# Kernel optimization log

Hardware: AMD Instinct MI355X
Metric: run time of the kernel (lower is better)

## Reference

```python
import jax, jax.numpy as jnp
import numpy as np
import math

D, NH, DFF = 1024, 16, 4096
B, S = 2, 2048
EPS = 1e-5


def _mha(q_in, k_in, v_in, wq, bq, wk, bk, wv, bv, wo, bo, mask):
    Bq, Sq, Dm = q_in.shape
    Sk = k_in.shape[1]
    dh = Dm // NH
    q = (q_in @ wq + bq).reshape(Bq, Sq, NH, dh).transpose(0, 2, 1, 3)
    k = (k_in @ wk + bk).reshape(Bq, Sk, NH, dh).transpose(0, 2, 1, 3)
    v = (v_in @ wv + bv).reshape(Bq, Sk, NH, dh).transpose(0, 2, 1, 3)
    scores = jnp.einsum('bhqd,bhkd->bhqk', q, k) / math.sqrt(dh)
    scores = jnp.where(mask == 0, jnp.float32(-1e9), scores)
    w = jax.nn.softmax(scores, axis=-1)
    out = jnp.einsum('bhqk,bhkd->bhqd', w, v)
    out = out.transpose(0, 2, 1, 3).reshape(Bq, Sq, Dm)
    return out @ wo + bo


def _ln(x, g, b):
    mu = jnp.mean(x, axis=-1, keepdims=True)
    var = jnp.var(x, axis=-1, keepdims=True)
    return (x - mu) * jax.lax.rsqrt(var + EPS) * g + b


def setup_inputs() -> dict:
    key = jax.random.key(0)
    ks = jax.random.split(key, 20)
    sc = 1.0 / math.sqrt(D)
    inp = {
        'x': jax.random.normal(ks[0], (B, S, D), jnp.float32),
        'encoder_output': jax.random.normal(ks[1], (B, S, D), jnp.float32),
        'src_mask': jnp.ones((B, 1, 1, S), jnp.int32),
        'tgt_mask': jnp.tril(jnp.ones((S, S), jnp.int32))[None, None],
    }
    names = ['s_wq', 's_wk', 's_wv', 's_wo', 'c_wq', 'c_wk', 'c_wv', 'c_wo']
    for i, n in enumerate(names):
        inp[n] = jax.random.normal(ks[2 + i], (D, D), jnp.float32) * sc
        inp[n.replace('w', 'b')] = jnp.zeros((D,), jnp.float32)
    inp['ff_w1'] = jax.random.normal(ks[10], (D, DFF), jnp.float32) * sc
    inp['ff_b1'] = jnp.zeros((DFF,), jnp.float32)
    inp['ff_w2'] = jax.random.normal(ks[11], (DFF, D), jnp.float32) / math.sqrt(DFF)
    inp['ff_b2'] = jnp.zeros((D,), jnp.float32)
    for i in (1, 2, 3):
        inp[f'ln{i}_g'] = jnp.ones((D,), jnp.float32)
        inp[f'ln{i}_b'] = jnp.zeros((D,), jnp.float32)
    return inp


def reference(x, encoder_output, src_mask, tgt_mask,
              s_wq, s_bq, s_wk, s_bk, s_wv, s_bv, s_wo, s_bo,
              c_wq, c_bq, c_wk, c_bk, c_wv, c_bv, c_wo, c_bo,
              ff_w1, ff_b1, ff_w2, ff_b2,
              ln1_g, ln1_b, ln2_g, ln2_b, ln3_g, ln3_b):
    # self-attention + residual + LN (dropout is identity in eval)
    a = _mha(x, x, x, s_wq, s_bq, s_wk, s_bk, s_wv, s_bv, s_wo, s_bo, tgt_mask)
    x = _ln(x + a, ln1_g, ln1_b)
    # cross-attention
    a = _mha(x, encoder_output, encoder_output,
             c_wq, c_bq, c_wk, c_bk, c_wv, c_bv, c_wo, c_bo, src_mask)
    x = _ln(x + a, ln2_g, ln2_b)
    # FFN
    f = jax.nn.relu(x @ ff_w1 + ff_b1) @ ff_w2 + ff_b2
    return _ln(x + f, ln3_g, ln3_b)
```

## Files before the change

kernel.cpp:

```cpp
#include <hip/hip_runtime.h>
#include <hip/hip_bf16.h>
#include <stdint.h>


#define DEV static __device__ __forceinline__

typedef short bf16s;
typedef __attribute__((ext_vector_type(8))) short bf16x8;
typedef __attribute__((ext_vector_type(4))) float f32x4;

DEV short f2b(float f) {
    union { __hip_bfloat16 h; short s; } u;
    u.h = __float2bfloat16(f);
    return u.s;
}

DEV unsigned pk2(float lo, float hi) {
    union { __hip_bfloat162 h; unsigned u; } u;
    u.h = __float22bfloat162_rn(float2{lo, hi});
    return u.u;
}

DEV f32x4 mfma16(bf16x8 a, bf16x8 b, f32x4 c) {
    return __builtin_amdgcn_mfma_f32_16x16x32_bf16(a, b, c, 0, 0, 0);
}

DEV void gload_lds16(const bf16s* g, short* l) {
    __builtin_amdgcn_global_load_lds(
        (const __attribute__((address_space(1))) void*)g,
        (__attribute__((address_space(3))) void*)l,
        16, 0, 0);
}

__global__ __launch_bounds__(256) void cast2_f32_bf16_kernel(
    const float* __restrict__ a, const float* __restrict__ b,
    bf16s* __restrict__ out, int n)
{
    int i = (blockIdx.x * 256 + threadIdx.x) * 8;
    const float* src = (i < n) ? a : b;
    int j = (i < n) ? i : i - n;
    const float4 u = *(const float4*)(src + j);
    const float4 v = *(const float4*)(src + j + 4);
    bf16x8 r;
    r[0] = f2b(u.x); r[1] = f2b(u.y); r[2] = f2b(u.z); r[3] = f2b(u.w);
    r[4] = f2b(v.x); r[5] = f2b(v.y); r[6] = f2b(v.z); r[7] = f2b(v.w);
    *(bf16x8*)(out + i) = r;
}

struct P8 { const float* p[8]; };

__global__ __launch_bounds__(256) void transpose_cast8_kernel(
    P8 srcs, bf16s* __restrict__ dst)
{
    __shared__ short tile[64][65];
    const float* W = srcs.p[blockIdx.z];
    bf16s* Wt = dst + (size_t)blockIdx.z * 1024 * 1024;
    const int n0 = blockIdx.x * 64, k0 = blockIdx.y * 64;
    const int t = threadIdx.x;
#pragma unroll
    for (int it = 0; it < 16; ++it) {
        int idx = it * 256 + t;
        int r = idx >> 6, c = idx & 63;
        tile[r][c] = f2b(W[(size_t)(k0 + r) * 1024 + n0 + c]);
    }
    __syncthreads();
#pragma unroll
    for (int it = 0; it < 16; ++it) {
        int idx = it * 256 + t;
        int r = idx >> 6, c = idx & 63;
        Wt[(size_t)(n0 + r) * 1024 + k0 + c] = tile[c][r];
    }
}

__global__ __launch_bounds__(256) void transpose_cast_kernel(
    const float* __restrict__ W, bf16s* __restrict__ Wt, int Krows, int Ncols)
{
    __shared__ short tile[64][65];
    const int n0 = blockIdx.x * 64, k0 = blockIdx.y * 64;
    const int t = threadIdx.x;
#pragma unroll
    for (int it = 0; it < 16; ++it) {
        int idx = it * 256 + t;
        int r = idx >> 6, c = idx & 63;
        tile[r][c] = f2b(W[(size_t)(k0 + r) * Ncols + n0 + c]);
    }
    __syncthreads();
#pragma unroll
    for (int it = 0; it < 16; ++it) {
        int idx = it * 256 + t;
        int r = idx >> 6, c = idx & 63;
        Wt[(size_t)(n0 + r) * Krows + k0 + c] = tile[c][r];
    }
}

__global__ __launch_bounds__(256) void transpose_v_kernel(
    const bf16s* __restrict__ V, int ldv, bf16s* __restrict__ Vt, int Sk)
{
    __shared__ short tile[64][65];
    const int s0 = blockIdx.x * 64;
    const int bh = blockIdx.y, b = bh >> 4, h = bh & 15;
    const int t = threadIdx.x;
#pragma unroll
    for (int it = 0; it < 16; ++it) {
        int idx = it * 256 + t;
        int r = idx >> 6, c = idx & 63;
        tile[r][c] = V[(size_t)(b * Sk + s0 + r) * ldv + h * 64 + c];
    }
    __syncthreads();
#pragma unroll
    for (int it = 0; it < 16; ++it) {
        int idx = it * 256 + t;
        int r = idx >> 6, c = idx & 63;
        Vt[((size_t)bh * 64 + r) * Sk + s0 + c] = tile[c][r];
    }
}

__global__ void concat3_kernel(const float* a, const float* b, const float* c,
                               float* o, int n)
{
    int i = blockIdx.x * 256 + threadIdx.x;
    if (i < n) { o[i] = a[i]; o[n + i] = b[i]; o[2 * n + i] = c[i]; }
}
__global__ void concat2_kernel(const float* a, const float* b, float* o, int n)
{
    int i = blockIdx.x * 256 + threadIdx.x;
    if (i < n) { o[i] = a[i]; o[n + i] = b[i]; }
}

template<int BM, int OUT_BF16, int RELU>
__global__ __launch_bounds__(256, (BM == 64 ? 4 : 2))
void gemm_bt_kernel(const bf16s* __restrict__ A, const bf16s* __restrict__ Bt,
                    const float* __restrict__ bias, void* __restrict__ Cp,
                    int M, int N, int K)
{
    constexpr int BN = 128;
    constexpr int WR = BM / 64;
    constexpr int WC = 4 / WR;
    constexpr int TN = BN / WC;
    constexpr int NF = TN / 16;
    constexpr int RA = BM / 64;
    constexpr int ASZ = BM * 32;

    __shared__ short As[2 * ASZ];
    __shared__ short Bs[2 * BN * 32];

    const int t = threadIdx.x, lane = t & 63, wave = t >> 6;
    const int g = lane >> 4, ln16 = lane & 15;
    const int wr = wave / WC, wc = wave % WC;
    const int rowA0 = blockIdx.y * BM, rowB0 = blockIdx.x * BN;

    const bf16s* Ab = A + (size_t)rowA0 * K;
    const bf16s* Bb = Bt + (size_t)rowB0 * K;

    f32x4 acc[4][NF] = {};

    auto stage = [&](int buf, int k0) {
        short* Ad = As + buf * ASZ;
        short* Bd = Bs + buf * BN * 32;
#pragma unroll
        for (int rnd = 0; rnd < RA; ++rnd) {
            int p = rnd * 256 + t;
            int sr = p >> 3, c3 = (p & 7) ^ (sr & 7);
            int r = sr * 2 + (c3 >> 2), c = c3 & 3;
            gload_lds16(Ab + (size_t)r * K + k0 + c * 8,
                        Ad + (rnd * 256 + wave * 64) * 8);
        }
#pragma unroll
        for (int rnd = 0; rnd < 2; ++rnd) {
            int p = rnd * 256 + t;
            int sr = p >> 3, c3 = (p & 7) ^ (sr & 7);
            int r = sr * 2 + (c3 >> 2), c = c3 & 3;
            gload_lds16(Bb + (size_t)r * K + k0 + c * 8,
                        Bd + (rnd * 256 + wave * 64) * 8);
        }
    };

    stage(0, 0);
    __syncthreads();
    int cur = 0;
    for (int k0 = 0; k0 < K; k0 += 32) {
        if (k0 + 32 < K) stage(cur ^ 1, k0 + 32);
        const short* Ar = As + cur * ASZ;
        const short* Br = Bs + cur * BN * 32;
        bf16x8 af[4], bfr[NF];
#pragma unroll
        for (int m = 0; m < 4; ++m) {
            int r = wr * 64 + m * 16 + ln16;
            int sr = r >> 1, c3 = (r & 1) * 4 + g;
            af[m] = *(const bf16x8*)(Ar + sr * 64 + ((c3 ^ (sr & 7)) * 8));
        }
#pragma unroll
        for (int n = 0; n < NF; ++n) {
            int r = wc * TN + n * 16 + ln16;
            int sr = r >> 1, c3 = (r & 1) * 4 + g;
            bfr[n] = *(const bf16x8*)(Br + sr * 64 + ((c3 ^ (sr & 7)) * 8));
        }
#pragma unroll
        for (int m = 0; m < 4; ++m)
#pragma unroll
            for (int n = 0; n < NF; ++n)
                acc[m][n] = mfma16(af[m], bfr[n], acc[m][n]);
        __syncthreads();
        cur ^= 1;
    }

    const int row0 = rowA0 + wr * 64, col0 = rowB0 + wc * TN;
#pragma unroll
    for (int n = 0; n < NF; ++n) {
        const int col = col0 + n * 16 + ln16;
        const float bv = bias[col];
#pragma unroll
        for (int m = 0; m < 4; ++m) {
#pragma unroll
            for (int r = 0; r < 4; ++r) {
                int row = row0 + m * 16 + g * 4 + r;
                float v = acc[m][n][r] + bv;
                if (RELU) v = fmaxf(v, 0.f);
                if (OUT_BF16) ((bf16s*)Cp)[(size_t)row * N + col] = f2b(v);
                else          ((float*)Cp)[(size_t)row * N + col] = v;
            }
        }
    }
}

template<int CAUSAL>
__global__ __launch_bounds__(256, 4)
void flash_kernel(const bf16s* __restrict__ Q, int ldq,
                  const bf16s* __restrict__ K, int ldk,
                  const bf16s* __restrict__ Vt,
                  bf16s* __restrict__ O, int ldo,
                  int Sq, int Sk, float scale)
{
    __shared__ short Ks[2 * 64 * 64];
    __shared__ short Vs[2 * 64 * 64];
    __shared__ short Ps[4 * 16 * 64];
    const int t = threadIdx.x, lane = t & 63, wave = t >> 6;
    const int g = lane >> 4, ln16 = lane & 15;
    const int qt = CAUSAL ? (int)(gridDim.x - 1 - blockIdx.x) : (int)blockIdx.x;
    const int bh = blockIdx.y, b = bh >> 4, h = bh & 15;
    const int q0 = qt * 64;
    const float sc2 = scale * 1.44269504f;

    bf16x8 aq[2];
    {
        const size_t qrow = (size_t)(b * Sq + q0 + wave * 16 + ln16);
#pragma unroll
        for (int kk = 0; kk < 2; ++kk)
            aq[kk] = *(const bf16x8*)(Q + qrow * ldq + h * 64 + kk * 32 + g * 8);
    }

    float m_raw = -1e30f, l_sum = 0.f;
    f32x4 oa[4] = {};

    const int nkt = CAUSAL ? (qt + 1) : (Sk >> 6);
    const bf16s* Kbase = K + (size_t)b * Sk * ldk + h * 64;
    const bf16s* Vbase = Vt + (size_t)bh * 64 * Sk;
    short* myP = Ps + wave * 1024;

    auto stage = [&](int buf, int kt) {
        const bf16s* ksrc = Kbase + (size_t)(kt * 64) * ldk;
        const bf16s* vsrc = Vbase + kt * 64;
        short* Kd = Ks + buf * 4096;
        short* Vd = Vs + buf * 4096;
#pragma unroll
        for (int rnd = 0; rnd < 2; ++rnd) {
            int p = rnd * 256 + t;
            int r = p >> 3, c = (p & 7) ^ (r & 7);
            gload_lds16(ksrc + (size_t)r * ldk + c * 8,
                        Kd + (rnd * 256 + wave * 64) * 8);
        }
#pragma unroll
        for (int rnd = 0; rnd < 2; ++rnd) {
            int p = rnd * 256 + t;
            int r = p >> 3, c = (p & 7) ^ (r & 7);
            gload_lds16(vsrc + (size_t)r * Sk + c * 8,
                        Vd + (rnd * 256 + wave * 64) * 8);
        }
    };

    stage(0, 0);
    __syncthreads();
    int cur = 0;

    for (int kt = 0; kt < nkt; ++kt) {
        if (kt + 1 < nkt) stage(cur ^ 1, kt + 1);
        const short* Kr = Ks + cur * 4096;
        const short* Vr = Vs + cur * 4096;

        f32x4 sa[4] = {};
        __builtin_amdgcn_s_setprio(1);
#pragma unroll
        for (int kk = 0; kk < 2; ++kk) {
#pragma unroll
            for (int n = 0; n < 4; ++n) {
                int key = n * 16 + ln16;
                bf16x8 ak = *(const bf16x8*)(Kr + key * 64 +
                                             (((kk * 4 + g) ^ (key & 7)) * 8));
                sa[n] = mfma16(ak, aq[kk], sa[n]);
            }
        }
        __builtin_amdgcn_s_setprio(0);

        float sv[4][4];
        const bool diag = CAUSAL && (kt == qt);
#pragma unroll
        for (int n = 0; n < 4; ++n)
#pragma unroll
            for (int r = 0; r < 4; ++r) {
                float s = sa[n][r];
                if (diag && (n * 16 + g * 4 + r > wave * 16 + ln16)) s = -1e30f;
                sv[n][r] = s;
            }

        float rm = fmaxf(
            fmaxf(fmaxf(fmaxf(sv[0][0], sv[0][1]), fmaxf(sv[0][2], sv[0][3])),
                  fmaxf(fmaxf(sv[1][0], sv[1][1]), fmaxf(sv[1][2], sv[1][3]))),
            fmaxf(fmaxf(fmaxf(sv[2][0], sv[2][1]), fmaxf(sv[2][2], sv[2][3])),
                  fmaxf(fmaxf(sv[3][0], sv[3][1]), fmaxf(sv[3][2], sv[3][3]))));
        rm = fmaxf(rm, __shfl_xor(rm, 16, 64));
        rm = fmaxf(rm, __shfl_xor(rm, 32, 64));

        const float mnew = fmaxf(m_raw, rm);
        const float al = exp2f((m_raw - mnew) * sc2);
        m_raw = mnew;
        const float nm = -mnew * sc2;

        float rs = 0.f;
#pragma unroll
        for (int n = 0; n < 4; ++n)
#pragma unroll
            for (int r = 0; r < 4; ++r) {
                float p = exp2f(fmaf(sv[n][r], sc2, nm));
                sv[n][r] = p;
                rs += p;
            }
        rs += __shfl_xor(rs, 16, 64);
        rs += __shfl_xor(rs, 32, 64);
        l_sum = l_sum * al + rs;

        float alr[4];
#pragma unroll
        for (int r = 0; r < 4; ++r)
            alr[r] = __shfl(al, g * 4 + r, 64);
#pragma unroll
        for (int n = 0; n < 4; ++n)
#pragma unroll
            for (int r = 0; r < 4; ++r)
                oa[n][r] *= alr[r];

#pragma unroll
        for (int n = 0; n < 4; ++n) {
            uint2 w;
            w.x = pk2(sv[n][0], sv[n][1]);
            w.y = pk2(sv[n][2], sv[n][3]);
            int c = n * 2 + (g >> 1);
            int sh = ln16 * 64 + ((c ^ (ln16 & 7)) * 8) + (g & 1) * 4;
            *(uint2*)(myP + sh) = w;
        }
        asm volatile("s_waitcnt lgkmcnt(0)" ::: "memory");

        __builtin_amdgcn_s_setprio(1);
#pragma unroll
        for (int kk = 0; kk < 2; ++kk) {
            bf16x8 pa = *(const bf16x8*)(myP + ln16 * 64 +
                                         (((kk * 4 + g) ^ (ln16 & 7)) * 8));
#pragma unroll
            for (int n = 0; n < 4; ++n) {
                int d = n * 16 + ln16;
                bf16x8 vb = *(const bf16x8*)(Vr + d * 64 +
                                             (((kk * 4 + g) ^ (d & 7)) * 8));
                oa[n] = mfma16(pa, vb, oa[n]);
            }
        }
        __builtin_amdgcn_s_setprio(0);
        __syncthreads();
        cur ^= 1;
    }

    const float inv = 1.f / l_sum;
    float invr[4];
#pragma unroll
    for (int r = 0; r < 4; ++r)
        invr[r] = __shfl(inv, g * 4 + r, 64);
#pragma unroll
    for (int n = 0; n < 4; ++n)
#pragma unroll
        for (int r = 0; r < 4; ++r) {
            int q = q0 + wave * 16 + g * 4 + r;
            int d = h * 64 + n * 16 + ln16;
            O[(size_t)(b * Sq + q) * ldo + d] = f2b(oa[n][r] * invr[r]);
        }
}

template<int WRITE_BF16>
__global__ __launch_bounds__(256)
void add_ln_kernel(const float* __restrict__ X, const float* __restrict__ A,
                   const float* __restrict__ G, const float* __restrict__ Bb,
                   float* __restrict__ Y, bf16s* __restrict__ Yb)
{
    const int row = blockIdx.x, t = threadIdx.x;
    const int lane = t & 63, w = t >> 6;
    const size_t base = (size_t)row * 1024 + t * 4;
    const float4 xv = *(const float4*)(X + base);
    const float4 av = *(const float4*)(A + base);
    float4 v;
    v.x = xv.x + av.x; v.y = xv.y + av.y; v.z = xv.z + av.z; v.w = xv.w + av.w;
    float s = v.x + v.y + v.z + v.w;
    float q = v.x * v.x + v.y * v.y + v.z * v.z + v.w * v.w;
#pragma unroll
    for (int x = 1; x < 64; x <<= 1) {
        s += __shfl_xor(s, x, 64);
        q += __shfl_xor(q, x, 64);
    }
    __shared__ float red[8];
    if (lane == 0) { red[w] = s; red[4 + w] = q; }
    __syncthreads();
    s = red[0] + red[1] + red[2] + red[3];
    q = red[4] + red[5] + red[6] + red[7];
    const float mu = s * (1.f / 1024.f);
    const float var = q * (1.f / 1024.f) - mu * mu;
    const float rstd = rsqrtf(var + 1e-5f);
    const float4 gv = *(const float4*)(G + t * 4);
    const float4 bv = *(const float4*)(Bb + t * 4);
    float o0 = (v.x - mu) * rstd * gv.x + bv.x;
    float o1 = (v.y - mu) * rstd * gv.y + bv.y;
    float o2 = (v.z - mu) * rstd * gv.z + bv.z;
    float o3 = (v.w - mu) * rstd * gv.w + bv.w;
    float4 ov; ov.x = o0; ov.y = o1; ov.z = o2; ov.w = o3;
    *(float4*)(Y + base) = ov;
    if (WRITE_BF16) {
        short4 yb;
        yb.x = f2b(o0); yb.y = f2b(o1); yb.z = f2b(o2); yb.w = f2b(o3);
        *(short4*)(Yb + base) = yb;
    }
}

extern "C" void kernel_launch(void* const* d_in, const int* in_sizes, int n_in,
                              void* d_out, int out_size, void* d_ws, size_t ws_size,
                              hipStream_t stream)
{
    constexpr int Dm = 1024, DFF = 4096, Bq = 2, S = 2048;
    constexpr int NT = Bq * S;
    constexpr size_t MM = (size_t)Dm * Dm;

    const float* x    = (const float*)d_in[0];
    const float* enc  = (const float*)d_in[1];
    const float* s_wq = (const float*)d_in[4];  const float* s_bq = (const float*)d_in[5];
    const float* s_wk = (const float*)d_in[6];  const float* s_bk = (const float*)d_in[7];
    const float* s_wv = (const float*)d_in[8];  const float* s_bv = (const float*)d_in[9];
    const float* s_wo = (const float*)d_in[10]; const float* s_bo = (const float*)d_in[11];
    const float* c_wq = (const float*)d_in[12]; const float* c_bq = (const float*)d_in[13];
    const float* c_wk = (const float*)d_in[14]; const float* c_bk = (const float*)d_in[15];
    const float* c_wv = (const float*)d_in[16]; const float* c_bv = (const float*)d_in[17];
    const float* c_wo = (const float*)d_in[18]; const float* c_bo = (const float*)d_in[19];
    const float* ffw1 = (const float*)d_in[20]; const float* ffb1 = (const float*)d_in[21];
    const float* ffw2 = (const float*)d_in[22]; const float* ffb2 = (const float*)d_in[23];
    const float* ln1g = (const float*)d_in[24]; const float* ln1b = (const float*)d_in[25];
    const float* ln2g = (const float*)d_in[26]; const float* ln2b = (const float*)d_in[27];
    const float* ln3g = (const float*)d_in[28]; const float* ln3b = (const float*)d_in[29];

    char* ws = (char*)d_ws;
    size_t off = 0;
    auto alloc = [&](size_t bytes) -> char* {
        char* p = ws + off;
        off += (bytes + 255) & ~(size_t)255;
        return p;
    };

    bf16s* xbf   = (bf16s*)alloc((size_t)NT * Dm * 2);
    bf16s* encbf = (bf16s*)alloc((size_t)NT * Dm * 2);
    bf16s* wAll  = (bf16s*)alloc(8 * MM * 2);
    bf16s* w1T   = (bf16s*)alloc((size_t)Dm * DFF * 2);
    bf16s* w2T   = (bf16s*)alloc((size_t)Dm * DFF * 2);
    float* bqkv  = (float*)alloc((size_t)3 * Dm * 4);
    float* bkvc  = (float*)alloc((size_t)2 * Dm * 4);
    bf16s* QKV   = (bf16s*)alloc((size_t)NT * 3 * Dm * 2);
    bf16s* Vt    = (bf16s*)alloc((size_t)NT * Dm * 2);
    bf16s* AO    = (bf16s*)alloc((size_t)NT * Dm * 2);
    float* Pbuf  = (float*)alloc((size_t)NT * Dm * 4);
    float* x1f   = (float*)alloc((size_t)NT * Dm * 4);
    bf16s* x1bf  = (bf16s*)alloc((size_t)NT * Dm * 2);
    float* x2f   = (float*)alloc((size_t)NT * Dm * 4);
    bf16s* x2bf  = (bf16s*)alloc((size_t)NT * Dm * 2);
    bf16s* Hbuf  = (bf16s*)alloc((size_t)NT * DFF * 2);
    (void)ws_size; (void)in_sizes; (void)n_in; (void)out_size;

    bf16s* wqkvT = wAll;
    bf16s* woTs  = wAll + 3 * MM;
    bf16s* wqTc  = wAll + 4 * MM;
    bf16s* wkvTc = wAll + 5 * MM;
    bf16s* woTc  = wAll + 7 * MM;

    cast2_f32_bf16_kernel<<<2 * NT * Dm / 8 / 256, 256, 0, stream>>>(
        x, enc, xbf, NT * Dm);
    P8 srcs = {{s_wq, s_wk, s_wv, s_wo, c_wq, c_wk, c_wv, c_wo}};
    transpose_cast8_kernel<<<dim3(16, 16, 8), 256, 0, stream>>>(srcs, wAll);
    transpose_cast_kernel<<<dim3(64, 16), 256, 0, stream>>>(ffw1, w1T, Dm, DFF);
    transpose_cast_kernel<<<dim3(16, 64), 256, 0, stream>>>(ffw2, w2T, DFF, Dm);
    concat3_kernel<<<4, 256, 0, stream>>>(s_bq, s_bk, s_bv, bqkv, Dm);
    concat2_kernel<<<4, 256, 0, stream>>>(c_bk, c_bv, bkvc, Dm);

    gemm_bt_kernel<128, 1, 0><<<dim3(24, 32), 256, 0, stream>>>(
        xbf, wqkvT, bqkv, QKV, NT, 3 * Dm, Dm);
    transpose_v_kernel<<<dim3(32, 32), 256, 0, stream>>>(
        QKV + 2 * Dm, 3 * Dm, Vt, S);
    flash_kernel<1><<<dim3(32, 32), 256, 0, stream>>>(
        QKV, 3 * Dm, QKV + Dm, 3 * Dm, Vt, AO, Dm, S, S, 0.125f);
    gemm_bt_kernel<64, 0, 0><<<dim3(8, 64), 256, 0, stream>>>(
        AO, woTs, s_bo, Pbuf, NT, Dm, Dm);
    add_ln_kernel<1><<<NT, 256, 0, stream>>>(x, Pbuf, ln1g, ln1b, x1f, x1bf);

    bf16s* Q2  = QKV;
    bf16s* KV2 = QKV + (size_t)NT * Dm;
    gemm_bt_kernel<64, 1, 0><<<dim3(8, 64), 256, 0, stream>>>(
        x1bf, wqTc, c_bq, Q2, NT, Dm, Dm);
    gemm_bt_kernel<128, 1, 0><<<dim3(16, 32), 256, 0, stream>>>(
        encbf, wkvTc, bkvc, KV2, NT, 2 * Dm, Dm);
    transpose_v_kernel<<<dim3(32, 32), 256, 0, stream>>>(
        KV2 + Dm, 2 * Dm, Vt, S);
    flash_kernel<0><<<dim3(32, 32), 256, 0, stream>>>(
        Q2, Dm, KV2, 2 * Dm, Vt, AO, Dm, S, S, 0.125f);
    gemm_bt_kernel<64, 0, 0><<<dim3(8, 64), 256, 0, stream>>>(
        AO, woTc, c_bo, Pbuf, NT, Dm, Dm);
    add_ln_kernel<1><<<NT, 256, 0, stream>>>(x1f, Pbuf, ln2g, ln2b, x2f, x2bf);

    gemm_bt_kernel<128, 1, 1><<<dim3(32, 32), 256, 0, stream>>>(
        x2bf, w1T, ffb1, Hbuf, NT, DFF, Dm);
    gemm_bt_kernel<64, 0, 0><<<dim3(8, 64), 256, 0, stream>>>(
        Hbuf, w2T, ffb2, Pbuf, NT, Dm, DFF);
    add_ln_kernel<0><<<NT, 256, 0, stream>>>(
        x2f, Pbuf, ln3g, ln3b, (float*)d_out, nullptr);
}
```

Baseline: 625.6 us.

## Remap flash grid to XCD-aware 1D order, lazy softmax rescale, fix P LDS conflicts

The flash attention grid becomes 1D and is remapped so that consecutive blocks sent to each of the 8 XCDs share the same batch-head, which is meant to improve L2 reuse of K/V. Online softmax now skips the max update and accumulator rescaling unless some row's max grows by more than a threshold (8 in log2 units), removing shuffles and multiplies on most iterations. The threshold keeps exponents bounded, at a small risk of overflow-related precision loss. The P tile LDS layout gets an extra half-swizzle, with reads split into two 64-bit loads, to reduce bank conflicts.

```diff
diff --git a/kernel.cpp b/kernel.cpp
--- a/kernel.cpp
+++ b/kernel.cpp
@@ -236,10 +236,19 @@
     __shared__ short Ps[4 * 16 * 64];
     const int t = threadIdx.x, lane = t & 63, wave = t >> 6;
     const int g = lane >> 4, ln16 = lane & 15;
-    const int qt = CAUSAL ? (int)(gridDim.x - 1 - blockIdx.x) : (int)blockIdx.x;
-    const int bh = blockIdx.y, b = bh >> 4, h = bh & 15;
+
+    const int nqt = Sq >> 6;
+    const int id = blockIdx.x;
+    const int perx = gridDim.x >> 3;
+    const int bhPerX = perx / nqt;
+    const int idx = id >> 3;
+    const int bh = (id & 7) * bhPerX + idx / nqt;
+    int qt = idx % nqt;
+    if (CAUSAL) qt = nqt - 1 - qt;
+    const int b = bh >> 4, h = bh & 15;
     const int q0 = qt * 64;
     const float sc2 = scale * 1.44269504f;
+    const float thrRaw = 8.0f / sc2;
 
     bf16x8 aq[2];
     {
@@ -320,10 +329,22 @@
         rm = fmaxf(rm, __shfl_xor(rm, 16, 64));
         rm = fmaxf(rm, __shfl_xor(rm, 32, 64));
 
-        const float mnew = fmaxf(m_raw, rm);
-        const float al = exp2f((m_raw - mnew) * sc2);
-        m_raw = mnew;
-        const float nm = -mnew * sc2;
+        if (!__all(rm <= m_raw + thrRaw)) {
+            const float mnew = fmaxf(m_raw, rm);
+            const float al = exp2f((m_raw - mnew) * sc2);
+            m_raw = mnew;
+            l_sum *= al;
+            float alr[4];
+#pragma unroll
+            for (int r = 0; r < 4; ++r)
+                alr[r] = __shfl(al, g * 4 + r, 64);
+#pragma unroll
+            for (int n = 0; n < 4; ++n)
+#pragma unroll
+                for (int r = 0; r < 4; ++r)
+                    oa[n][r] *= alr[r];
+        }
+        const float nm = -m_raw * sc2;
 
         float rs = 0.f;
 #pragma unroll
@@ -336,17 +357,7 @@
             }
         rs += __shfl_xor(rs, 16, 64);
         rs += __shfl_xor(rs, 32, 64);
-        l_sum = l_sum * al + rs;
-
-        float alr[4];
-#pragma unroll
-        for (int r = 0; r < 4; ++r)
-            alr[r] = __shfl(al, g * 4 + r, 64);
-#pragma unroll
-        for (int n = 0; n < 4; ++n)
-#pragma unroll
-            for (int r = 0; r < 4; ++r)
-                oa[n][r] *= alr[r];
+        l_sum += rs;
 
 #pragma unroll
         for (int n = 0; n < 4; ++n) {
@@ -354,7 +365,8 @@
             w.x = pk2(sv[n][0], sv[n][1]);
             w.y = pk2(sv[n][2], sv[n][3]);
             int c = n * 2 + (g >> 1);
-            int sh = ln16 * 64 + ((c ^ (ln16 & 7)) * 8) + (g & 1) * 4;
+            int sh = ln16 * 64 + ((c ^ (ln16 & 7)) * 8) +
+                     (((g & 1) ^ (ln16 >> 3)) * 4);
             *(uint2*)(myP + sh) = w;
         }
         asm volatile("s_waitcnt lgkmcnt(0)" ::: "memory");
@@ -362,8 +374,12 @@
         __builtin_amdgcn_s_setprio(1);
 #pragma unroll
         for (int kk = 0; kk < 2; ++kk) {
-            bf16x8 pa = *(const bf16x8*)(myP + ln16 * 64 +
-                                         (((kk * 4 + g) ^ (ln16 & 7)) * 8));
+            const int base = ln16 * 64 + (((kk * 4 + g) ^ (ln16 & 7)) * 8);
+            const int x0 = (ln16 >> 3) * 4;
+            union { bf16x8 v; uint2 u2[2]; } pu;
+            pu.u2[0] = *(const uint2*)(myP + base + x0);
+            pu.u2[1] = *(const uint2*)(myP + base + (x0 ^ 4));
+            bf16x8 pa = pu.v;
 #pragma unroll
             for (int n = 0; n < 4; ++n) {
                 int d = n * 16 + ln16;
@@ -504,7 +520,7 @@
         xbf, wqkvT, bqkv, QKV, NT, 3 * Dm, Dm);
     transpose_v_kernel<<<dim3(32, 32), 256, 0, stream>>>(
         QKV + 2 * Dm, 3 * Dm, Vt, S);
-    flash_kernel<1><<<dim3(32, 32), 256, 0, stream>>>(
+    flash_kernel<1><<<dim3(1024), 256, 0, stream>>>(
         QKV, 3 * Dm, QKV + Dm, 3 * Dm, Vt, AO, Dm, S, S, 0.125f);
     gemm_bt_kernel<64, 0, 0><<<dim3(8, 64), 256, 0, stream>>>(
         AO, woTs, s_bo, Pbuf, NT, Dm, Dm);
@@ -518,7 +534,7 @@
         encbf, wkvTc, bkvc, KV2, NT, 2 * Dm, Dm);
     transpose_v_kernel<<<dim3(32, 32), 256, 0, stream>>>(
         KV2 + Dm, 2 * Dm, Vt, S);
-    flash_kernel<0><<<dim3(32, 32), 256, 0, stream>>>(
+    flash_kernel<0><<<dim3(1024), 256, 0, stream>>>(
         Q2, Dm, KV2, 2 * Dm, Vt, AO, Dm, S, S, 0.125f);
     gemm_bt_kernel<64, 0, 0><<<dim3(8, 64), 256, 0, stream>>>(
         AO, woTc, c_bo, Pbuf, NT, Dm, Dm);
```

Measured after the change: 627.5 us. Within noise of the previous version (+0.3%).
